# Optimization experiments

Measured on AMD Instinct MI355X. Metric: run time of the kernel, lower is better.

Reference implementation:

```python
import jax, jax.numpy as jnp
import numpy as np

SIM_THRESHOLD = 0.7
EPS = 1e-8  # matches torch F.cosine_similarity eps

Q, M, D, C = 4096, 65536, 384, 128


def setup_inputs() -> dict:
    key = jax.random.key(0)
    k1, k2, k3 = jax.random.split(key, 3)
    query_embeddings = jax.random.normal(k1, (Q, D), dtype=jnp.float32)
    memory_embeddings = jax.random.normal(k2, (M, D), dtype=jnp.float32)
    # per-example one-hot-ish label vectors [M, C]
    memory_labels = jax.random.uniform(k3, (M, C), dtype=jnp.float32)
    return {
        "query_embeddings": query_embeddings,
        "memory_embeddings": memory_embeddings,
        "memory_labels": memory_labels,
    }


def _l2_normalize(x):
    n = jnp.sqrt(jnp.sum(x * x, axis=-1, keepdims=True))
    return x / jnp.maximum(n, EPS)


def reference(query_embeddings, memory_embeddings, memory_labels):
    # cosine similarity matrix [Q, M] via normalized GEMM
    qn = _l2_normalize(query_embeddings)          # [Q, D]
    mn = _l2_normalize(memory_embeddings)         # [M, D]
    sims = jnp.einsum("qd,md->qm", qn, mn)        # [Q, M]
    max_sim = jnp.max(sims, axis=1)               # [Q]
    max_idx = jnp.argmax(sims, axis=1)            # [Q]
    picked = memory_labels[max_idx]               # [Q, C] gather
    C_ = memory_labels.shape[1]
    uniform = jnp.full((1, C_), 1.0 / C_, dtype=picked.dtype)
    predictions = jnp.where((max_sim > SIM_THRESHOLD)[:, None], picked, uniform)
    return predictions
```

## Files before the change

### kernel.cpp

```cpp
#include <hip/hip_runtime.h>
#include <math.h>

#define QN 4096
#define MN 65536
#define DN 384
#define CN 128
#define NCHUNK 64
#define MROWS_PER_CHUNK (MN / NCHUNK)
#define MT_PER (MROWS_PER_CHUNK / 64)
#define BTILE_B (64 * DN)

typedef __attribute__((ext_vector_type(8))) int i32x8;
typedef __attribute__((ext_vector_type(4))) int i32x4;
typedef __attribute__((ext_vector_type(4))) float f32x4;

__device__ __forceinline__ unsigned char f2fp8(float f) {
  return (unsigned char)(__builtin_amdgcn_cvt_pk_fp8_f32(f, 0.f, 0, false) & 0xff);
}

__device__ __forceinline__ void async16(const void* g, void* l) {
  __builtin_amdgcn_global_load_lds(
      (const __attribute__((address_space(1))) unsigned int*)g,
      (__attribute__((address_space(3))) unsigned int*)l, 16, 0, 0);
}

__global__ __launch_bounds__(256) void nrm_kernel(const float* __restrict__ qe,
                                                  const float* __restrict__ me,
                                                  unsigned char* __restrict__ yq,
                                                  unsigned char* __restrict__ ym) {
  const int row = blockIdx.x * 4 + (threadIdx.x >> 6);
  const int lane = threadIdx.x & 63;
  const float* xr;
  unsigned char* yr;
  if (row < QN) {
    xr = qe + (size_t)row * DN;
    yr = yq + (size_t)row * DN;
  } else {
    xr = me + (size_t)(row - QN) * DN;
    yr = ym + (size_t)(row - QN) * DN;
  }
  float v[6];
  float ss = 0.f;
#pragma unroll
  for (int i = 0; i < 6; ++i) {
    v[i] = xr[lane + i * 64];
    ss += v[i] * v[i];
  }
#pragma unroll
  for (int m = 1; m < 64; m <<= 1) ss += __shfl_xor(ss, m);
  const float scale = 1.0f / fmaxf(sqrtf(ss), 1e-8f);
#pragma unroll
  for (int i = 0; i < 6; ++i) yr[lane + i * 64] = f2fp8(v[i] * scale);
}

__global__ __launch_bounds__(256, 2) void gemm_max_kernel(
    const unsigned char* __restrict__ qn8, const unsigned char* __restrict__ mn8,
    float* __restrict__ pmax) {
  __shared__ unsigned char Bs[2 * BTILE_B];
  __shared__ float smax[2][128];

  const int tid = threadIdx.x;
  const int wave = tid >> 6, lane = tid & 63;
  const int wr = wave >> 1, wc = wave & 1;
  const int quad = lane >> 4, l16 = lane & 15;
  const int r7 = l16 & 7;
  const int qrow0 = blockIdx.x * 128;
  const int mchunk0 = blockIdx.y * MROWS_PER_CHUNK;

  float rmax[16];
#pragma unroll
  for (int i = 0; i < 16; ++i) rmax[i] = -3.0e38f;

  {
    const unsigned char* abase = qn8 + (size_t)qrow0 * DN;
#pragma unroll
    for (int i = 0; i < 12; ++i) {
      const int ci = i * 256 + tid;
      const int row = ci / 24;
      const int j = ci - row * 24;
      const int gj = (j & 24) | ((j ^ row) & 7);
      async16(abase + row * DN + gj * 16, &Bs[(i * 256 + wave * 64) * 16]);
    }
  }
  __syncthreads();
  i32x8 afr[3][4];
#pragma unroll
  for (int kc = 0; kc < 3; ++kc)
#pragma unroll
    for (int rt = 0; rt < 4; ++rt) {
      const unsigned char* p = &Bs[(wr * 64 + rt * 16 + l16) * DN];
      i32x4 lo = *(const i32x4*)&p[(kc * 8 + ((quad * 2 + 0) ^ r7)) * 16];
      i32x4 hi = *(const i32x4*)&p[(kc * 8 + ((quad * 2 + 1) ^ r7)) * 16];
      afr[kc][rt][0] = lo[0]; afr[kc][rt][1] = lo[1];
      afr[kc][rt][2] = lo[2]; afr[kc][rt][3] = lo[3];
      afr[kc][rt][4] = hi[0]; afr[kc][rt][5] = hi[1];
      afr[kc][rt][6] = hi[2]; afr[kc][rt][7] = hi[3];
    }
  __syncthreads();

  int srcoff[6];
#pragma unroll
  for (int i = 0; i < 6; ++i) {
    const int ci = i * 256 + tid;
    const int row = ci / 24;
    const int j = ci - row * 24;
    const int gj = (j & 24) | ((j ^ row) & 7);
    srcoff[i] = row * DN + gj * 16;
  }

  const unsigned char* bchunk = mn8 + (size_t)mchunk0 * DN;
#pragma unroll
  for (int i = 0; i < 6; ++i)
    async16(bchunk + srcoff[i], &Bs[(i * 256 + wave * 64) * 16]);

  const int c_lo = ((quad * 2 + 0) ^ r7) * 16;
  const int c_hi = ((quad * 2 + 1) ^ r7) * 16;

#pragma unroll 1
  for (int mt = 0; mt < MT_PER; ++mt) {
    __syncthreads();
    const unsigned char* cur = &Bs[(mt & 1) * BTILE_B];
    if (mt + 1 < MT_PER) {
      unsigned char* nxt = &Bs[((mt + 1) & 1) * BTILE_B];
      const unsigned char* nb = bchunk + (size_t)(mt + 1) * BTILE_B;
#pragma unroll
      for (int i = 0; i < 6; ++i)
        async16(nb + srcoff[i], &nxt[(i * 256 + wave * 64) * 16]);
    }

    f32x4 acc[4][2];
#pragma unroll
    for (int rt = 0; rt < 4; ++rt)
#pragma unroll
      for (int ct = 0; ct < 2; ++ct) acc[rt][ct] = (f32x4){0.f, 0.f, 0.f, 0.f};

    i32x8 bfr[2][2];
#pragma unroll
    for (int ct = 0; ct < 2; ++ct) {
      const unsigned char* p = &cur[(wc * 32 + ct * 16 + l16) * DN];
      i32x4 lo = *(const i32x4*)&p[c_lo];
      i32x4 hi = *(const i32x4*)&p[c_hi];
      bfr[0][ct][0] = lo[0]; bfr[0][ct][1] = lo[1];
      bfr[0][ct][2] = lo[2]; bfr[0][ct][3] = lo[3];
      bfr[0][ct][4] = hi[0]; bfr[0][ct][5] = hi[1];
      bfr[0][ct][6] = hi[2]; bfr[0][ct][7] = hi[3];
    }
#pragma unroll
    for (int kc = 0; kc < 3; ++kc) {
      const int pb = kc & 1;
      if (kc < 2) {
#pragma unroll
        for (int ct = 0; ct < 2; ++ct) {
          const unsigned char* p =
              &cur[(wc * 32 + ct * 16 + l16) * DN + (kc + 1) * 128];
          i32x4 lo = *(const i32x4*)&p[c_lo];
          i32x4 hi = *(const i32x4*)&p[c_hi];
          bfr[pb ^ 1][ct][0] = lo[0]; bfr[pb ^ 1][ct][1] = lo[1];
          bfr[pb ^ 1][ct][2] = lo[2]; bfr[pb ^ 1][ct][3] = lo[3];
          bfr[pb ^ 1][ct][4] = hi[0]; bfr[pb ^ 1][ct][5] = hi[1];
          bfr[pb ^ 1][ct][6] = hi[2]; bfr[pb ^ 1][ct][7] = hi[3];
        }
      }
#pragma unroll
      for (int rt = 0; rt < 4; ++rt)
#pragma unroll
        for (int ct = 0; ct < 2; ++ct)
          acc[rt][ct] = __builtin_amdgcn_mfma_scale_f32_16x16x128_f8f6f4(
              afr[kc][rt], bfr[pb][ct], acc[rt][ct], 0, 0,
              0, 0x7f7f7f7f, 0, 0x7f7f7f7f);
    }

#pragma unroll
    for (int rt = 0; rt < 4; ++rt)
#pragma unroll
      for (int r = 0; r < 4; ++r) {
        const float v = fmaxf(acc[rt][0][r], acc[rt][1][r]);
        rmax[rt * 4 + r] = fmaxf(rmax[rt * 4 + r], v);
      }
  }

#pragma unroll
  for (int i = 0; i < 16; ++i) {
    float v = rmax[i];
    v = fmaxf(v, __shfl_xor(v, 1));
    v = fmaxf(v, __shfl_xor(v, 2));
    v = fmaxf(v, __shfl_xor(v, 4));
    v = fmaxf(v, __shfl_xor(v, 8));
    rmax[i] = v;
  }
  if (l16 == 0) {
#pragma unroll
    for (int rt = 0; rt < 4; ++rt)
#pragma unroll
      for (int r = 0; r < 4; ++r)
        smax[wc][wr * 64 + rt * 16 + quad * 4 + r] = rmax[rt * 4 + r];
  }
  __syncthreads();
  if (tid < 128) {
    const float v = fmaxf(smax[0][tid], smax[1][tid]);
    pmax[(size_t)(qrow0 + tid) * NCHUNK + blockIdx.y] = v;
  }
}

__global__ __launch_bounds__(256) void decide_kernel(
    const float* __restrict__ pmax, const float* __restrict__ qe,
    const float* __restrict__ me, const float* __restrict__ labels,
    float* __restrict__ out) {
  const int q = blockIdx.x;
  const int t = threadIdx.x;
  __shared__ float smx;
  if (t < 64) {
    float v = pmax[(size_t)q * NCHUNK + t];
#pragma unroll
    for (int m = 1; m < 64; m <<= 1) v = fmaxf(v, __shfl_xor(v, m));
    if (t == 0) smx = v;
  }
  __syncthreads();
  if (smx <= 0.5f) {
    if (t < CN) out[(size_t)q * CN + t] = 1.0f / 128.0f;
    return;
  }
  __shared__ float sred[256];
  __shared__ int sidx[256];
  __shared__ float wsum[4];
  const float* qr = qe + (size_t)q * DN;
  float ss = 0.f;
  for (int i = t; i < DN; i += 256) ss += qr[i] * qr[i];
#pragma unroll
  for (int m = 1; m < 64; m <<= 1) ss += __shfl_xor(ss, m);
  if ((t & 63) == 0) wsum[t >> 6] = ss;
  __syncthreads();
  const float qnorm = fmaxf(sqrtf(wsum[0] + wsum[1] + wsum[2] + wsum[3]), 1e-8f);

  float best = -3.0e38f;
  int bidx = 0x7fffffff;
  for (int j = t; j < MN; j += 256) {
    const float* mr = me + (size_t)j * DN;
    float dot = 0.f, ms = 0.f;
    for (int k = 0; k < DN; ++k) {
      float a = qr[k], b = mr[k];
      dot += a * b;
      ms += b * b;
    }
    const float sim = dot / (qnorm * fmaxf(sqrtf(ms), 1e-8f));
    if (sim > best) { best = sim; bidx = j; }
  }
  sred[t] = best;
  sidx[t] = bidx;
  __syncthreads();
  for (int s = 128; s > 0; s >>= 1) {
    if (t < s) {
      const float ov = sred[t + s];
      const int oi = sidx[t + s];
      if (ov > sred[t] || (ov == sred[t] && oi < sidx[t])) {
        sred[t] = ov;
        sidx[t] = oi;
      }
    }
    __syncthreads();
  }
  const float mx = sred[0];
  const int mi = sidx[0];
  if (t < CN)
    out[(size_t)q * CN + t] =
        (mx > 0.7f) ? labels[(size_t)mi * CN + t] : (1.0f / 128.0f);
}

extern "C" void kernel_launch(void* const* d_in, const int* in_sizes, int n_in,
                              void* d_out, int out_size, void* d_ws,
                              size_t ws_size, hipStream_t stream) {
  const float* qe = (const float*)d_in[0];
  const float* me = (const float*)d_in[1];
  const float* lb = (const float*)d_in[2];
  float* out = (float*)d_out;

  char* ws = (char*)d_ws;
  const size_t OFF_QN = 0;
  const size_t OFF_MN = OFF_QN + (size_t)QN * DN;
  const size_t OFF_PMAX = OFF_MN + (size_t)MN * DN;
  unsigned char* qn8 = (unsigned char*)(ws + OFF_QN);
  unsigned char* mn8 = (unsigned char*)(ws + OFF_MN);
  float* pmax = (float*)(ws + OFF_PMAX);

  nrm_kernel<<<(QN + MN) / 4, 256, 0, stream>>>(qe, me, qn8, mn8);
  gemm_max_kernel<<<dim3(QN / 128, NCHUNK), 256, 0, stream>>>(qn8, mn8, pmax);
  decide_kernel<<<QN, 256, 0, stream>>>(pmax, qe, me, lb, out);
}
```

Measured before the change: 254.5 us.

## Pad LDS rows to 400 bytes, remap blocks per XCD, preload all B fragments

Replaces the XOR-swizzled LDS layout with rows padded to 400 bytes (25 16-byte chunks), filling the pad chunk with a dummy load, so fragment reads avoid bank conflicts without swizzle arithmetic. Blocks are remapped so each XCD handles its own set of memory chunks across all query tiles, aiming for better L2 reuse of the B operand. The inner loop now loads all three k-chunks of B fragments up front instead of double-buffering them in registers. In exchange it uses more LDS per block and more registers, which could lower occupancy, and it adds extra async copies for the padding.

```diff
diff --git a/kernel.cpp b/kernel.cpp
--- a/kernel.cpp
+++ b/kernel.cpp
@@ -8,7 +8,11 @@
 #define NCHUNK 64
 #define MROWS_PER_CHUNK (MN / NCHUNK)
 #define MT_PER (MROWS_PER_CHUNK / 64)
-#define BTILE_B (64 * DN)
+
+#define LROW 400
+#define LCHUNKS 25
+#define BTILE_B (64 * LROW)
+#define GTILE_B (64 * DN)
 
 typedef __attribute__((ext_vector_type(8))) int i32x8;
 typedef __attribute__((ext_vector_type(4))) int i32x4;
@@ -63,9 +67,13 @@
   const int wave = tid >> 6, lane = tid & 63;
   const int wr = wave >> 1, wc = wave & 1;
   const int quad = lane >> 4, l16 = lane & 15;
-  const int r7 = l16 & 7;
-  const int qrow0 = blockIdx.x * 128;
-  const int mchunk0 = blockIdx.y * MROWS_PER_CHUNK;
+
+  const int bid = blockIdx.y * gridDim.x + blockIdx.x;
+  const int xcd = bid & 7;
+  const int j = bid >> 3;
+  const int ychunk = (xcd << 3) | (j >> 5);
+  const int qrow0 = (j & 31) * 128;
+  const int mchunk0 = ychunk * MROWS_PER_CHUNK;
 
   float rmax[16];
 #pragma unroll
@@ -76,10 +84,17 @@
 #pragma unroll
     for (int i = 0; i < 12; ++i) {
       const int ci = i * 256 + tid;
-      const int row = ci / 24;
-      const int j = ci - row * 24;
-      const int gj = (j & 24) | ((j ^ row) & 7);
-      async16(abase + row * DN + gj * 16, &Bs[(i * 256 + wave * 64) * 16]);
+      const int row = ci / LCHUNKS;
+      const int c16 = ci - row * LCHUNKS;
+      const int sc = (c16 < 24) ? c16 : 0;
+      async16(abase + row * DN + sc * 16, &Bs[(i * 256 + wave * 64) * 16]);
+    }
+    if (wave < 2) {
+      const int ci = 3072 + wave * 64 + lane;
+      const int row = ci / LCHUNKS;
+      const int c16 = ci - row * LCHUNKS;
+      const int sc = (c16 < 24) ? c16 : 0;
+      async16(abase + row * DN + sc * 16, &Bs[(3072 + wave * 64) * 16]);
     }
   }
   __syncthreads();
@@ -88,9 +103,9 @@
   for (int kc = 0; kc < 3; ++kc)
 #pragma unroll
     for (int rt = 0; rt < 4; ++rt) {
-      const unsigned char* p = &Bs[(wr * 64 + rt * 16 + l16) * DN];
-      i32x4 lo = *(const i32x4*)&p[(kc * 8 + ((quad * 2 + 0) ^ r7)) * 16];
-      i32x4 hi = *(const i32x4*)&p[(kc * 8 + ((quad * 2 + 1) ^ r7)) * 16];
+      const unsigned char* p = &Bs[(wr * 64 + rt * 16 + l16) * LROW + kc * 128];
+      i32x4 lo = *(const i32x4*)&p[(quad * 2 + 0) * 16];
+      i32x4 hi = *(const i32x4*)&p[(quad * 2 + 1) * 16];
       afr[kc][rt][0] = lo[0]; afr[kc][rt][1] = lo[1];
       afr[kc][rt][2] = lo[2]; afr[kc][rt][3] = lo[3];
       afr[kc][rt][4] = hi[0]; afr[kc][rt][5] = hi[1];
@@ -98,23 +113,31 @@
     }
   __syncthreads();
 
-  int srcoff[6];
+  int srcoff[7];
 #pragma unroll
   for (int i = 0; i < 6; ++i) {
     const int ci = i * 256 + tid;
-    const int row = ci / 24;
-    const int j = ci - row * 24;
-    const int gj = (j & 24) | ((j ^ row) & 7);
-    srcoff[i] = row * DN + gj * 16;
+    const int row = ci / LCHUNKS;
+    const int c16 = ci - row * LCHUNKS;
+    const int sc = (c16 < 24) ? c16 : 0;
+    srcoff[i] = row * DN + sc * 16;
+  }
+  {
+    const int ci = 1536 + lane;
+    const int row = ci / LCHUNKS;
+    const int c16 = ci - row * LCHUNKS;
+    const int sc = (c16 < 24) ? c16 : 0;
+    srcoff[6] = row * DN + sc * 16;
   }
 
   const unsigned char* bchunk = mn8 + (size_t)mchunk0 * DN;
 #pragma unroll
   for (int i = 0; i < 6; ++i)
     async16(bchunk + srcoff[i], &Bs[(i * 256 + wave * 64) * 16]);
-
-  const int c_lo = ((quad * 2 + 0) ^ r7) * 16;
-  const int c_hi = ((quad * 2 + 1) ^ r7) * 16;
+  if (wave == 0) async16(bchunk + srcoff[6], &Bs[1536 * 16]);
+
+  const int c_lo = (quad * 2 + 0) * 16;
+  const int c_hi = (quad * 2 + 1) * 16;
 
 #pragma unroll 1
   for (int mt = 0; mt < MT_PER; ++mt) {
@@ -122,11 +145,27 @@
     const unsigned char* cur = &Bs[(mt & 1) * BTILE_B];
     if (mt + 1 < MT_PER) {
       unsigned char* nxt = &Bs[((mt + 1) & 1) * BTILE_B];
-      const unsigned char* nb = bchunk + (size_t)(mt + 1) * BTILE_B;
+      const unsigned char* nb = bchunk + (size_t)(mt + 1) * GTILE_B;
 #pragma unroll
       for (int i = 0; i < 6; ++i)
         async16(nb + srcoff[i], &nxt[(i * 256 + wave * 64) * 16]);
-    }
+      if (wave == 0) async16(nb + srcoff[6], &nxt[1536 * 16]);
+    }
+
+    i32x8 bfr[3][2];
+#pragma unroll
+    for (int kc = 0; kc < 3; ++kc)
+#pragma unroll
+      for (int ct = 0; ct < 2; ++ct) {
+        const unsigned char* p =
+            &cur[(wc * 32 + ct * 16 + l16) * LROW + kc * 128];
+        i32x4 lo = *(const i32x4*)&p[c_lo];
+        i32x4 hi = *(const i32x4*)&p[c_hi];
+        bfr[kc][ct][0] = lo[0]; bfr[kc][ct][1] = lo[1];
+        bfr[kc][ct][2] = lo[2]; bfr[kc][ct][3] = lo[3];
+        bfr[kc][ct][4] = hi[0]; bfr[kc][ct][5] = hi[1];
+        bfr[kc][ct][6] = hi[2]; bfr[kc][ct][7] = hi[3];
+      }
 
     f32x4 acc[4][2];
 #pragma unroll
@@ -134,41 +173,15 @@
 #pragma unroll
       for (int ct = 0; ct < 2; ++ct) acc[rt][ct] = (f32x4){0.f, 0.f, 0.f, 0.f};
 
-    i32x8 bfr[2][2];
-#pragma unroll
-    for (int ct = 0; ct < 2; ++ct) {
-      const unsigned char* p = &cur[(wc * 32 + ct * 16 + l16) * DN];
-      i32x4 lo = *(const i32x4*)&p[c_lo];
-      i32x4 hi = *(const i32x4*)&p[c_hi];
-      bfr[0][ct][0] = lo[0]; bfr[0][ct][1] = lo[1];
-      bfr[0][ct][2] = lo[2]; bfr[0][ct][3] = lo[3];
-      bfr[0][ct][4] = hi[0]; bfr[0][ct][5] = hi[1];
-      bfr[0][ct][6] = hi[2]; bfr[0][ct][7] = hi[3];
-    }
-#pragma unroll
-    for (int kc = 0; kc < 3; ++kc) {
-      const int pb = kc & 1;
-      if (kc < 2) {
-#pragma unroll
-        for (int ct = 0; ct < 2; ++ct) {
-          const unsigned char* p =
-              &cur[(wc * 32 + ct * 16 + l16) * DN + (kc + 1) * 128];
-          i32x4 lo = *(const i32x4*)&p[c_lo];
-          i32x4 hi = *(const i32x4*)&p[c_hi];
-          bfr[pb ^ 1][ct][0] = lo[0]; bfr[pb ^ 1][ct][1] = lo[1];
-          bfr[pb ^ 1][ct][2] = lo[2]; bfr[pb ^ 1][ct][3] = lo[3];
-          bfr[pb ^ 1][ct][4] = hi[0]; bfr[pb ^ 1][ct][5] = hi[1];
-          bfr[pb ^ 1][ct][6] = hi[2]; bfr[pb ^ 1][ct][7] = hi[3];
-        }
-      }
+#pragma unroll
+    for (int kc = 0; kc < 3; ++kc)
 #pragma unroll
       for (int rt = 0; rt < 4; ++rt)
 #pragma unroll
         for (int ct = 0; ct < 2; ++ct)
           acc[rt][ct] = __builtin_amdgcn_mfma_scale_f32_16x16x128_f8f6f4(
-              afr[kc][rt], bfr[pb][ct], acc[rt][ct], 0, 0,
+              afr[kc][rt], bfr[kc][ct], acc[rt][ct], 0, 0,
               0, 0x7f7f7f7f, 0, 0x7f7f7f7f);
-    }
 
 #pragma unroll
     for (int rt = 0; rt < 4; ++rt)
@@ -198,7 +211,7 @@
   __syncthreads();
   if (tid < 128) {
     const float v = fmaxf(smax[0][tid], smax[1][tid]);
-    pmax[(size_t)(qrow0 + tid) * NCHUNK + blockIdx.y] = v;
+    pmax[(size_t)(qrow0 + tid) * NCHUNK + ychunk] = v;
   }
 }
 
```

Measured after the change: 258.5 us. No clear change (+1.6%).

## Deepen B-tile prefetch to two tiles, split LDS read barrier, remap blocks per XCD

Applied to the files above, without the earlier changes.

Prefetches two memory tiles ahead using explicit vmcnt waits instead of a full __syncthreads. All B fragments for a tile are loaded into registers up front, then a second barrier frees that buffer so the next-but-one tile can be loaded while the MFMAs run at raised wave priority. Block IDs are also remapped so that each XCD works on a contiguous group of memory chunks, improving L2 reuse of the memory embeddings. The changes add register pressure from holding the full B fragment set and rely on hand-written waitcnt values matching the number of outstanding loads.

```diff
diff --git a/kernel.cpp b/kernel.cpp
--- a/kernel.cpp
+++ b/kernel.cpp
@@ -64,8 +64,13 @@
   const int wr = wave >> 1, wc = wave & 1;
   const int quad = lane >> 4, l16 = lane & 15;
   const int r7 = l16 & 7;
-  const int qrow0 = blockIdx.x * 128;
-  const int mchunk0 = blockIdx.y * MROWS_PER_CHUNK;
+
+  const int bid = blockIdx.y * gridDim.x + blockIdx.x;
+  const int xcd = bid & 7;
+  const int j = bid >> 3;
+  const int ychunk = (xcd << 3) | (j >> 5);
+  const int qrow0 = (j & 31) * 128;
+  const int mchunk0 = ychunk * MROWS_PER_CHUNK;
 
   float rmax[16];
 #pragma unroll
@@ -77,8 +82,8 @@
     for (int i = 0; i < 12; ++i) {
       const int ci = i * 256 + tid;
       const int row = ci / 24;
-      const int j = ci - row * 24;
-      const int gj = (j & 24) | ((j ^ row) & 7);
+      const int jj = ci - row * 24;
+      const int gj = (jj & 24) | ((jj ^ row) & 7);
       async16(abase + row * DN + gj * 16, &Bs[(i * 256 + wave * 64) * 16]);
     }
   }
@@ -103,8 +108,8 @@
   for (int i = 0; i < 6; ++i) {
     const int ci = i * 256 + tid;
     const int row = ci / 24;
-    const int j = ci - row * 24;
-    const int gj = (j & 24) | ((j ^ row) & 7);
+    const int jj = ci - row * 24;
+    const int gj = (jj & 24) | ((jj ^ row) & 7);
     srcoff[i] = row * DN + gj * 16;
   }
 
@@ -112,17 +117,43 @@
 #pragma unroll
   for (int i = 0; i < 6; ++i)
     async16(bchunk + srcoff[i], &Bs[(i * 256 + wave * 64) * 16]);
-
-  const int c_lo = ((quad * 2 + 0) ^ r7) * 16;
-  const int c_hi = ((quad * 2 + 1) ^ r7) * 16;
+#pragma unroll
+  for (int i = 0; i < 6; ++i)
+    async16(bchunk + BTILE_B + srcoff[i],
+            &Bs[BTILE_B + (i * 256 + wave * 64) * 16]);
 
 #pragma unroll 1
   for (int mt = 0; mt < MT_PER; ++mt) {
-    __syncthreads();
+    if (mt == MT_PER - 1)
+      asm volatile("s_waitcnt vmcnt(0)" ::: "memory");
+    else
+      asm volatile("s_waitcnt vmcnt(6)" ::: "memory");
+    __builtin_amdgcn_s_barrier();
+    __builtin_amdgcn_sched_barrier(0);
+
     const unsigned char* cur = &Bs[(mt & 1) * BTILE_B];
-    if (mt + 1 < MT_PER) {
-      unsigned char* nxt = &Bs[((mt + 1) & 1) * BTILE_B];
-      const unsigned char* nb = bchunk + (size_t)(mt + 1) * BTILE_B;
+
+    i32x8 bfr[3][2];
+#pragma unroll
+    for (int kc = 0; kc < 3; ++kc)
+#pragma unroll
+      for (int ct = 0; ct < 2; ++ct) {
+        const unsigned char* p = &cur[(wc * 32 + ct * 16 + l16) * DN];
+        i32x4 lo = *(const i32x4*)&p[(kc * 8 + ((quad * 2 + 0) ^ r7)) * 16];
+        i32x4 hi = *(const i32x4*)&p[(kc * 8 + ((quad * 2 + 1) ^ r7)) * 16];
+        bfr[kc][ct][0] = lo[0]; bfr[kc][ct][1] = lo[1];
+        bfr[kc][ct][2] = lo[2]; bfr[kc][ct][3] = lo[3];
+        bfr[kc][ct][4] = hi[0]; bfr[kc][ct][5] = hi[1];
+        bfr[kc][ct][6] = hi[2]; bfr[kc][ct][7] = hi[3];
+      }
+
+    asm volatile("s_waitcnt lgkmcnt(0)" ::: "memory");
+    __builtin_amdgcn_sched_barrier(0);
+    __builtin_amdgcn_s_barrier();
+
+    if (mt + 2 < MT_PER) {
+      unsigned char* nxt = (unsigned char*)cur;
+      const unsigned char* nb = bchunk + (size_t)(mt + 2) * BTILE_B;
 #pragma unroll
       for (int i = 0; i < 6; ++i)
         async16(nb + srcoff[i], &nxt[(i * 256 + wave * 64) * 16]);
@@ -134,41 +165,17 @@
 #pragma unroll
       for (int ct = 0; ct < 2; ++ct) acc[rt][ct] = (f32x4){0.f, 0.f, 0.f, 0.f};
 
-    i32x8 bfr[2][2];
-#pragma unroll
-    for (int ct = 0; ct < 2; ++ct) {
-      const unsigned char* p = &cur[(wc * 32 + ct * 16 + l16) * DN];
-      i32x4 lo = *(const i32x4*)&p[c_lo];
-      i32x4 hi = *(const i32x4*)&p[c_hi];
-      bfr[0][ct][0] = lo[0]; bfr[0][ct][1] = lo[1];
-      bfr[0][ct][2] = lo[2]; bfr[0][ct][3] = lo[3];
-      bfr[0][ct][4] = hi[0]; bfr[0][ct][5] = hi[1];
-      bfr[0][ct][6] = hi[2]; bfr[0][ct][7] = hi[3];
-    }
-#pragma unroll
-    for (int kc = 0; kc < 3; ++kc) {
-      const int pb = kc & 1;
-      if (kc < 2) {
-#pragma unroll
-        for (int ct = 0; ct < 2; ++ct) {
-          const unsigned char* p =
-              &cur[(wc * 32 + ct * 16 + l16) * DN + (kc + 1) * 128];
-          i32x4 lo = *(const i32x4*)&p[c_lo];
-          i32x4 hi = *(const i32x4*)&p[c_hi];
-          bfr[pb ^ 1][ct][0] = lo[0]; bfr[pb ^ 1][ct][1] = lo[1];
-          bfr[pb ^ 1][ct][2] = lo[2]; bfr[pb ^ 1][ct][3] = lo[3];
-          bfr[pb ^ 1][ct][4] = hi[0]; bfr[pb ^ 1][ct][5] = hi[1];
-          bfr[pb ^ 1][ct][6] = hi[2]; bfr[pb ^ 1][ct][7] = hi[3];
-        }
-      }
+    __builtin_amdgcn_s_setprio(1);
+#pragma unroll
+    for (int kc = 0; kc < 3; ++kc)
 #pragma unroll
       for (int rt = 0; rt < 4; ++rt)
 #pragma unroll
         for (int ct = 0; ct < 2; ++ct)
           acc[rt][ct] = __builtin_amdgcn_mfma_scale_f32_16x16x128_f8f6f4(
-              afr[kc][rt], bfr[pb][ct], acc[rt][ct], 0, 0,
+              afr[kc][rt], bfr[kc][ct], acc[rt][ct], 0, 0,
               0, 0x7f7f7f7f, 0, 0x7f7f7f7f);
-    }
+    __builtin_amdgcn_s_setprio(0);
 
 #pragma unroll
     for (int rt = 0; rt < 4; ++rt)
@@ -198,7 +205,7 @@
   __syncthreads();
   if (tid < 128) {
     const float v = fmaxf(smax[0][tid], smax[1][tid]);
-    pmax[(size_t)(qrow0 + tid) * NCHUNK + blockIdx.y] = v;
+    pmax[(size_t)(qrow0 + tid) * NCHUNK + ychunk] = v;
   }
 }
 
```

Result: faster. 246.6 us (-3.1%).
